# Kernel tuning notes

Hardware: AMD Instinct MI355X
Metric: run time of the kernel (lower is better)

## Reference

```python
import jax, jax.numpy as jnp
import numpy as np

N = 50000   # nodes
E = 800000  # edges (sparse adjacency nnz)
FI = 256    # input feature dim
FO = 64     # output feature dim per head
H = 8       # attention heads


def setup_inputs() -> dict:
    key = jax.random.key(0)
    ks = jax.random.split(key, 6)
    x = jax.random.normal(ks[0], (N, FI), dtype=jnp.float32)
    W = jax.random.normal(ks[1], (H, FI, FO), dtype=jnp.float32) * 0.05
    a = jax.random.normal(ks[2], (H, FO), dtype=jnp.float32) * 0.05
    b = jax.random.normal(ks[3], (H, FO), dtype=jnp.float32) * 0.05
    rows = jax.random.randint(ks[4], (E,), 0, N, dtype=jnp.int32)
    cols = jax.random.randint(ks[5], (E,), 0, N, dtype=jnp.int32)
    return {"x": x, "W": W, "a": a, "b": b, "rows": rows, "cols": cols}


def reference(x, W, a, b, rows, cols):
    # SparseGAT forward: per head linear -> edge scores -> sparse row softmax
    # -> sparse aggregation -> bias; heads averaged then ReLU.
    n = x.shape[0]
    h = W.shape[0]
    NEG_SLOPE = 0.2  # tf.nn.leaky_relu default alpha
    acc = None
    for i in range(h):  # small fixed loop over heads
        t = x @ W[i]                                   # [N, FO]
        aw = t @ a[i]                                  # [N]
        e = jax.nn.leaky_relu(aw[rows] + aw[cols], NEG_SLOPE)   # [E]
        # sparse softmax per row (segment softmax, numerically stable)
        m = jax.ops.segment_max(e, rows, num_segments=n)        # [N]
        ex = jnp.exp(e - m[rows])                                # [E]
        den = jax.ops.segment_sum(ex, rows, num_segments=n)      # [N]
        coef = ex / den[rows]                                    # [E]
        # sparse matmul: sum_j coef_ij * t_j
        agg = jax.ops.segment_sum(coef[:, None] * t[cols], rows, num_segments=n)
        agg = agg + b[i]
        acc = agg if acc is None else acc + agg
    return jax.nn.relu(acc / h)
```

## Files before the change

### kernel.cpp

```cpp
#include <hip/hip_runtime.h>
#include <hip/hip_bf16.h>


#define FI 256
#define FO 64
#define NH 8
#define FC (NH * FO)
#define TTP 528

typedef _Float16 f16x8 __attribute__((ext_vector_type(8)));
typedef float f32x16 __attribute__((ext_vector_type(16)));
typedef float f32x8 __attribute__((ext_vector_type(8)));

__global__ __launch_bounds__(256)
void p1_wconv(const float* __restrict__ W, _Float16* __restrict__ Wth) {
  int idx = blockIdx.x * 256 + threadIdx.x;
  if (idx >= NH * FO * FI) return;
  int k = idx & (FI - 1);
  int f = (idx >> 8) & (FO - 1);
  int h = idx >> 14;
  Wth[idx] = (_Float16)W[((size_t)h * FI + k) * FO + f];
}

__global__ __launch_bounds__(256)
void k1_fused(const float* __restrict__ x, const _Float16* __restrict__ Wth,
              const float* __restrict__ a, _Float16* __restrict__ Th2,
              float* __restrict__ aw, int N) {
  __shared__ _Float16 Xs[32][264];
  __shared__ _Float16 Tt[32][TTP];
  const int bm  = blockIdx.x * 32;
  const int t   = threadIdx.x;
  const int lane = t & 63;
  const int wid  = t >> 6;
  const int l31 = lane & 31;
  const int kh  = (lane >> 5) * 8;

  #pragma unroll
  for (int r = 0; r < 8; ++r) {
    int i = t + r * 256;
    int row = i >> 6;
    int q   = i & 63;
    int grow = bm + row;
    float4 v = make_float4(0.f, 0.f, 0.f, 0.f);
    if (grow < N)
      v = reinterpret_cast<const float4*>(&x[(size_t)grow * FI])[q];
    _Float16 o[4] = {(_Float16)v.x, (_Float16)v.y, (_Float16)v.z, (_Float16)v.w};
    *reinterpret_cast<uint2*>(&Xs[row][q * 4]) = *reinterpret_cast<uint2*>(o);
  }
  __syncthreads();

  #pragma unroll
  for (int hh = 0; hh < 2; ++hh) {
    const int h = wid * 2 + hh;
    #pragma unroll
    for (int wc = 0; wc < 2; ++wc) {
      const _Float16* Wcol = Wth + ((size_t)h * FO + wc * 32 + l31) * FI;
      f32x16 acc = (f32x16)0.0f;
      #pragma unroll
      for (int kk = 0; kk < 16; ++kk) {
        f16x8 af = *reinterpret_cast<const f16x8*>(&Xs[l31][kk * 16 + kh]);
        f16x8 bf = *reinterpret_cast<const f16x8*>(&Wcol[kk * 16 + kh]);
        acc = __builtin_amdgcn_mfma_f32_32x32x16_f16(af, bf, acc, 0, 0, 0);
      }
      const int f = wc * 32 + l31;
      #pragma unroll
      for (int reg = 0; reg < 16; ++reg) {
        int rr = (reg & 3) + 8 * (reg >> 2) + 4 * (lane >> 5);
        Tt[rr][f * NH + h] = (_Float16)acc[reg];
      }
    }
  }
  __syncthreads();

  float a_l[NH];
  #pragma unroll
  for (int h = 0; h < NH; ++h) a_l[h] = a[h * FO + lane];
  #pragma unroll
  for (int rr = 0; rr < 8; ++rr) {
    const int row = wid * 8 + rr;
    f16x8 v = *reinterpret_cast<const f16x8*>(&Tt[row][lane * NH]);
    float p[NH];
    #pragma unroll
    for (int h = 0; h < NH; ++h) p[h] = (float)v[h] * a_l[h];
    #pragma unroll
    for (int off = 1; off < 64; off <<= 1) {
      #pragma unroll
      for (int h = 0; h < NH; ++h) p[h] += __shfl_xor(p[h], off);
    }
    if (lane == 0 && bm + row < N) {
      f32x8 o;
      #pragma unroll
      for (int h = 0; h < NH; ++h) o[h] = p[h];
      *reinterpret_cast<f32x8*>(&aw[(size_t)(bm + row) * NH]) = o;
    }
  }

  #pragma unroll
  for (int r = 0; r < 8; ++r) {
    int i = t + r * 256;
    int row = i >> 6;
    int q   = i & 63;
    if (bm + row < N)
      reinterpret_cast<uint4*>(&Th2[(size_t)(bm + row) * FC])[q] =
          *reinterpret_cast<const uint4*>(&Tt[row][q * 8]);
  }
}

__global__ __launch_bounds__(256)
void b1_hist(const int* __restrict__ rows, int* __restrict__ deg, int E) {
  int e = blockIdx.x * 256 + threadIdx.x;
  if (e < E) atomicAdd(&deg[rows[e]], 1);
}

__global__ __launch_bounds__(256)
void b2a_blocksum(const int* __restrict__ deg, int* __restrict__ blocksums, int N) {
  __shared__ int red[256];
  const int t = threadIdx.x;
  const int base = blockIdx.x * 1024 + t * 4;
  int s = 0;
  #pragma unroll
  for (int j = 0; j < 4; ++j) { int i = base + j; if (i < N) s += deg[i]; }
  red[t] = s;
  __syncthreads();
  for (int off = 128; off; off >>= 1) {
    if (t < off) red[t] += red[t + off];
    __syncthreads();
  }
  if (t == 0) blocksums[blockIdx.x] = red[0];
}

__global__ __launch_bounds__(64)
void b2b_scanblocks(int* __restrict__ blocksums, int nb,
                    int* __restrict__ row_start, int N, int E) {
  const int lane = threadIdx.x;
  int carry = 0;
  for (int base = 0; base < nb; base += 64) {
    int i = base + lane;
    int v = (i < nb) ? blocksums[i] : 0;
    int inc = v;
    #pragma unroll
    for (int off = 1; off < 64; off <<= 1) {
      int t = __shfl_up(inc, off);
      if (lane >= off) inc += t;
    }
    if (i < nb) blocksums[i] = inc - v + carry;
    carry += __shfl(inc, 63);
  }
  if (lane == 0) row_start[N] = E;
}

__global__ __launch_bounds__(256)
void b2c_rescan(const int* __restrict__ deg, const int* __restrict__ blocksums,
                int* __restrict__ row_start, int* __restrict__ cursor, int N) {
  __shared__ int ts[256];
  const int t = threadIdx.x;
  const int base = blockIdx.x * 1024 + t * 4;
  int v[4]; int s = 0;
  #pragma unroll
  for (int j = 0; j < 4; ++j) { int i = base + j; v[j] = (i < N) ? deg[i] : 0; s += v[j]; }
  ts[t] = s;
  __syncthreads();
  for (int off = 1; off < 256; off <<= 1) {
    int add = (t >= off) ? ts[t - off] : 0;
    __syncthreads();
    ts[t] += add;
    __syncthreads();
  }
  int run = blocksums[blockIdx.x] + ts[t] - s;
  #pragma unroll
  for (int j = 0; j < 4; ++j) {
    int i = base + j;
    if (i < N) { row_start[i] = run; cursor[i] = run; run += v[j]; }
  }
}

__global__ __launch_bounds__(256)
void b3_scatter(const int* __restrict__ rows, const int* __restrict__ cols,
                int* __restrict__ cursor, int* __restrict__ colperm, int E) {
  int e = blockIdx.x * 256 + threadIdx.x;
  if (e >= E) return;
  int pos = atomicAdd(&cursor[rows[e]], 1);
  colperm[pos] = cols[e];
}

__global__ __launch_bounds__(256)
void k4_fused(const int* __restrict__ row_start, const int* __restrict__ colperm,
              const float* __restrict__ aw, const _Float16* __restrict__ Th2,
              const float* __restrict__ b, float* __restrict__ out, int N) {
  const int lane16 = threadIdx.x & 15;
  const int gbase  = threadIdx.x & 48;
  const int r = blockIdx.x * 16 + (threadIdx.x >> 4);
  if (r >= N) return;

  const int s0 = row_start[r], s1 = row_start[r + 1];

  f32x8 awr = *reinterpret_cast<const f32x8*>(&aw[(size_t)r * NH]);

  float facc[4][NH] = {};
  float dacc[NH] = {};

  for (int base = s0; base < s1; base += 16) {
    const int mm = min(16, s1 - base);
    const bool valid = lane16 < mm;
    int c_l = valid ? colperm[base + lane16] : 0;

    f32x8 awc = *reinterpret_cast<const f32x8*>(&aw[(size_t)c_l * NH]);
    float ex[NH];
    #pragma unroll
    for (int h = 0; h < NH; ++h) {
      float s = awr[h] + awc[h];
      float lr = s > 0.f ? s : 0.2f * s;
      ex[h] = valid ? __expf(lr) : 0.f;
      dacc[h] += ex[h];
    }

    for (int j = 0; j < mm; ++j) {
      int cj = __shfl(c_l, gbase + j);
      const _Float16* tp = Th2 + (size_t)cj * FC + lane16 * NH;
      f16x8 tv0 = *reinterpret_cast<const f16x8*>(tp);
      f16x8 tv1 = *reinterpret_cast<const f16x8*>(tp + 128);
      f16x8 tv2 = *reinterpret_cast<const f16x8*>(tp + 256);
      f16x8 tv3 = *reinterpret_cast<const f16x8*>(tp + 384);
      #pragma unroll
      for (int h = 0; h < NH; ++h) {
        float e = __shfl(ex[h], gbase + j);
        facc[0][h] = fmaf(e, (float)tv0[h], facc[0][h]);
        facc[1][h] = fmaf(e, (float)tv1[h], facc[1][h]);
        facc[2][h] = fmaf(e, (float)tv2[h], facc[2][h]);
        facc[3][h] = fmaf(e, (float)tv3[h], facc[3][h]);
      }
    }
  }

  #pragma unroll
  for (int h = 0; h < NH; ++h) {
    #pragma unroll
    for (int off = 1; off < 16; off <<= 1)
      dacc[h] += __shfl_xor(dacc[h], off);
  }

  float rden[NH];
  #pragma unroll
  for (int h = 0; h < NH; ++h) rden[h] = dacc[h] > 0.f ? 1.0f / dacc[h] : 0.f;

  #pragma unroll
  for (int q = 0; q < 4; ++q) {
    const int f = q * 16 + lane16;
    float sb = 0.f;
    #pragma unroll
    for (int h = 0; h < NH; ++h) sb += b[h * FO + f];
    float v = 0.f;
    #pragma unroll
    for (int h = 0; h < NH; ++h) v += facc[q][h] * rden[h];
    v = (v + sb) * 0.125f;
    out[(size_t)r * FO + f] = v > 0.f ? v : 0.f;
  }
}

extern "C" void kernel_launch(void* const* d_in, const int* in_sizes, int n_in,
                              void* d_out, int out_size, void* d_ws, size_t ws_size,
                              hipStream_t stream) {
  const float* x    = (const float*)d_in[0];
  const float* W    = (const float*)d_in[1];
  const float* a    = (const float*)d_in[2];
  const float* b    = (const float*)d_in[3];
  const int*   rows = (const int*)d_in[4];
  const int*   cols = (const int*)d_in[5];
  const int N = in_sizes[0] / FI;
  const int E = in_sizes[4];

  char* p = (char*)d_ws;
  _Float16* Th2      = (_Float16*)p;  p += (size_t)N * FC * sizeof(_Float16);
  _Float16* Wth      = (_Float16*)p;  p += (size_t)NH * FO * FI * sizeof(_Float16);
  float*    aw       = (float*)p;     p += (size_t)N * NH * sizeof(float);
  int*      deg      = (int*)p;       p += (size_t)N * sizeof(int);
  int*      row_start= (int*)p;       p += (size_t)(N + 4) * sizeof(int);
  int*      cursor   = (int*)p;       p += (size_t)N * sizeof(int);
  int*      colperm  = (int*)p;       p += (size_t)E * sizeof(int);
  int*      blocksums= (int*)p;       p += 64 * sizeof(int);
  float*    out = (float*)d_out;

  const int nb = (N + 1023) / 1024;

  hipMemsetAsync(deg, 0, (size_t)N * sizeof(int), stream);
  b1_hist<<<(E + 255) / 256, 256, 0, stream>>>(rows, deg, E);
  b2a_blocksum<<<nb, 256, 0, stream>>>(deg, blocksums, N);
  b2b_scanblocks<<<1, 64, 0, stream>>>(blocksums, nb, row_start, N, E);
  b2c_rescan<<<nb, 256, 0, stream>>>(deg, blocksums, row_start, cursor, N);
  b3_scatter<<<(E + 255) / 256, 256, 0, stream>>>(rows, cols, cursor, colperm, E);

  p1_wconv<<<(NH * FO * FI + 255) / 256, 256, 0, stream>>>(W, Wth);
  k1_fused<<<(N + 31) / 32, 256, 0, stream>>>(x, Wth, a, Th2, aw, N);

  k4_fused<<<(N + 15) / 16, 256, 0, stream>>>(row_start, colperm, aw, Th2, b, out, N);
}
```

Baseline: 314.6 us.

## Retile projection GEMM to 128-row blocks with per-head waves; prefetch gathers in aggregation

The projection kernel now handles 128 rows per block with 512 threads. Each wave owns one head and computes four 32-row MFMA tiles, so every W fragment load is reused across four row tiles, and K is staged in two halves to reduce shared memory. The attention logits come straight from the accumulators through lane shuffles rather than from an LDS re-read. The aggregation kernel stores edge exponentials in shared memory instead of shuffling them per head, and software-prefetches the next neighbour's feature row to hide gather latency, at the cost of more registers and extra LDS traffic.

New measurement: 292.6 us. 7.0% less time.

```diff
diff --git a/kernel.cpp b/kernel.cpp
--- a/kernel.cpp
+++ b/kernel.cpp
@@ -5,12 +5,13 @@
 #define FI 256
 #define FO 64
 #define NH 8
-#define FC (NH * FO)
-#define TTP 528
+#define FC 512
+#define BM 128
 
 typedef _Float16 f16x8 __attribute__((ext_vector_type(8)));
 typedef float f32x16 __attribute__((ext_vector_type(16)));
 typedef float f32x8 __attribute__((ext_vector_type(8)));
+typedef float f32x4 __attribute__((ext_vector_type(4)));
 
 __global__ __launch_bounds__(256)
 void p1_wconv(const float* __restrict__ W, _Float16* __restrict__ Wth) {
@@ -22,87 +23,97 @@
   Wth[idx] = (_Float16)W[((size_t)h * FI + k) * FO + f];
 }
 
-__global__ __launch_bounds__(256)
-void k1_fused(const float* __restrict__ x, const _Float16* __restrict__ Wth,
-              const float* __restrict__ a, _Float16* __restrict__ Th2,
-              float* __restrict__ aw, int N) {
-  __shared__ _Float16 Xs[32][264];
-  __shared__ _Float16 Tt[32][TTP];
-  const int bm  = blockIdx.x * 32;
-  const int t   = threadIdx.x;
+__global__ __launch_bounds__(512)
+void k1_v2(const float* __restrict__ x, const _Float16* __restrict__ Wth,
+           const float* __restrict__ a, _Float16* __restrict__ Th2,
+           float* __restrict__ aw, int N) {
+  __shared__ _Float16 smem[BM * 136];
+  auto Xs = reinterpret_cast<_Float16(*)[136]>(smem);
+  auto Tt = reinterpret_cast<_Float16(*)[512]>(smem);
+  const int bm = blockIdx.x * BM;
+  const int t = threadIdx.x;
+  const int w = t >> 6;
   const int lane = t & 63;
-  const int wid  = t >> 6;
   const int l31 = lane & 31;
-  const int kh  = (lane >> 5) * 8;
-
-  #pragma unroll
-  for (int r = 0; r < 8; ++r) {
-    int i = t + r * 256;
-    int row = i >> 6;
-    int q   = i & 63;
-    int grow = bm + row;
-    float4 v = make_float4(0.f, 0.f, 0.f, 0.f);
-    if (grow < N)
-      v = reinterpret_cast<const float4*>(&x[(size_t)grow * FI])[q];
-    _Float16 o[4] = {(_Float16)v.x, (_Float16)v.y, (_Float16)v.z, (_Float16)v.w};
-    *reinterpret_cast<uint2*>(&Xs[row][q * 4]) = *reinterpret_cast<uint2*>(o);
-  }
-  __syncthreads();
-
-  #pragma unroll
-  for (int hh = 0; hh < 2; ++hh) {
-    const int h = wid * 2 + hh;
+  const int kh = (lane >> 5) * 8;
+  const _Float16* Wh = Wth + (size_t)w * (FO * FI);
+
+  f32x16 acc[4][2];
+  #pragma unroll
+  for (int mr = 0; mr < 4; ++mr)
+    #pragma unroll
+    for (int wc = 0; wc < 2; ++wc) acc[mr][wc] = (f32x16)0.0f;
+
+  #pragma unroll
+  for (int k0 = 0; k0 < 2; ++k0) {
+    if (k0) __syncthreads();
+    #pragma unroll
+    for (int r = 0; r < 8; ++r) {
+      int i = t + r * 512;
+      int row = i >> 5;
+      int q = i & 31;
+      float4 v = make_float4(0.f, 0.f, 0.f, 0.f);
+      if (bm + row < N)
+        v = reinterpret_cast<const float4*>(&x[(size_t)(bm + row) * FI + k0 * 128])[q];
+      _Float16 o[4] = {(_Float16)v.x, (_Float16)v.y, (_Float16)v.z, (_Float16)v.w};
+      *reinterpret_cast<uint2*>(&Xs[row][q * 4]) = *reinterpret_cast<uint2*>(o);
+    }
+    __syncthreads();
+    #pragma unroll
+    for (int kk = 0; kk < 8; ++kk) {
+      f16x8 af[4], bf[2];
+      #pragma unroll
+      for (int mr = 0; mr < 4; ++mr)
+        af[mr] = *reinterpret_cast<const f16x8*>(&Xs[mr * 32 + l31][kk * 16 + kh]);
+      #pragma unroll
+      for (int wc = 0; wc < 2; ++wc)
+        bf[wc] = *reinterpret_cast<const f16x8*>(
+            &Wh[(size_t)(wc * 32 + l31) * FI + k0 * 128 + kk * 16 + kh]);
+      #pragma unroll
+      for (int mr = 0; mr < 4; ++mr)
+        #pragma unroll
+        for (int wc = 0; wc < 2; ++wc)
+          acc[mr][wc] =
+              __builtin_amdgcn_mfma_f32_32x32x16_f16(af[mr], bf[wc], acc[mr][wc], 0, 0, 0);
+    }
+  }
+
+  const float av0 = a[w * FO + l31], av1 = a[w * FO + 32 + l31];
+  #pragma unroll
+  for (int mr = 0; mr < 4; ++mr)
+    #pragma unroll
+    for (int reg = 0; reg < 16; ++reg) {
+      float s = acc[mr][0][reg] * av0 + acc[mr][1][reg] * av1;
+      #pragma unroll
+      for (int off = 1; off < 32; off <<= 1) s += __shfl_xor(s, off);
+      if (l31 == 0) {
+        int rl = mr * 32 + (reg & 3) + 8 * (reg >> 2) + 4 * (lane >> 5);
+        if (bm + rl < N) aw[(size_t)(bm + rl) * NH + w] = s;
+      }
+    }
+
+  #pragma unroll
+  for (int ch = 0; ch < 4; ++ch) {
+    __syncthreads();
     #pragma unroll
     for (int wc = 0; wc < 2; ++wc) {
-      const _Float16* Wcol = Wth + ((size_t)h * FO + wc * 32 + l31) * FI;
-      f32x16 acc = (f32x16)0.0f;
-      #pragma unroll
-      for (int kk = 0; kk < 16; ++kk) {
-        f16x8 af = *reinterpret_cast<const f16x8*>(&Xs[l31][kk * 16 + kh]);
-        f16x8 bf = *reinterpret_cast<const f16x8*>(&Wcol[kk * 16 + kh]);
-        acc = __builtin_amdgcn_mfma_f32_32x32x16_f16(af, bf, acc, 0, 0, 0);
+      const int f = wc * 32 + l31;
+      #pragma unroll
+      for (int reg = 0; reg < 16; ++reg) {
+        int rl = (reg & 3) + 8 * (reg >> 2) + 4 * (lane >> 5);
+        Tt[rl][f * NH + w] = (_Float16)acc[ch][wc][reg];
       }
-      const int f = wc * 32 + l31;
-      #pragma unroll
-      for (int reg = 0; reg < 16; ++reg) {
-        int rr = (reg & 3) + 8 * (reg >> 2) + 4 * (lane >> 5);
-        Tt[rr][f * NH + h] = (_Float16)acc[reg];
-      }
-    }
-  }
-  __syncthreads();
-
-  float a_l[NH];
-  #pragma unroll
-  for (int h = 0; h < NH; ++h) a_l[h] = a[h * FO + lane];
-  #pragma unroll
-  for (int rr = 0; rr < 8; ++rr) {
-    const int row = wid * 8 + rr;
-    f16x8 v = *reinterpret_cast<const f16x8*>(&Tt[row][lane * NH]);
-    float p[NH];
-    #pragma unroll
-    for (int h = 0; h < NH; ++h) p[h] = (float)v[h] * a_l[h];
-    #pragma unroll
-    for (int off = 1; off < 64; off <<= 1) {
-      #pragma unroll
-      for (int h = 0; h < NH; ++h) p[h] += __shfl_xor(p[h], off);
-    }
-    if (lane == 0 && bm + row < N) {
-      f32x8 o;
-      #pragma unroll
-      for (int h = 0; h < NH; ++h) o[h] = p[h];
-      *reinterpret_cast<f32x8*>(&aw[(size_t)(bm + row) * NH]) = o;
-    }
-  }
-
-  #pragma unroll
-  for (int r = 0; r < 8; ++r) {
-    int i = t + r * 256;
-    int row = i >> 6;
-    int q   = i & 63;
-    if (bm + row < N)
-      reinterpret_cast<uint4*>(&Th2[(size_t)(bm + row) * FC])[q] =
-          *reinterpret_cast<const uint4*>(&Tt[row][q * 8]);
+    }
+    __syncthreads();
+    #pragma unroll
+    for (int r = 0; r < 4; ++r) {
+      int i = t + r * 512;
+      int row = i >> 6, q = i & 63;
+      int grow = bm + ch * 32 + row;
+      if (grow < N)
+        *reinterpret_cast<uint4*>(&Th2[(size_t)grow * FC + q * 8]) =
+            *reinterpret_cast<const uint4*>(&Tt[row][q * 8]);
+    }
   }
 }
 
@@ -187,13 +198,15 @@
 void k4_fused(const int* __restrict__ row_start, const int* __restrict__ colperm,
               const float* __restrict__ aw, const _Float16* __restrict__ Th2,
               const float* __restrict__ b, float* __restrict__ out, int N) {
+  __shared__ float exs[16][132];
   const int lane16 = threadIdx.x & 15;
+  const int g      = threadIdx.x >> 4;
   const int gbase  = threadIdx.x & 48;
-  const int r = blockIdx.x * 16 + (threadIdx.x >> 4);
+  const int r = blockIdx.x * 16 + g;
   if (r >= N) return;
+  float* exg = &exs[g][0];
 
   const int s0 = row_start[r], s1 = row_start[r + 1];
-
   f32x8 awr = *reinterpret_cast<const f32x8*>(&aw[(size_t)r * NH]);
 
   float facc[4][NH] = {};
@@ -205,30 +218,45 @@
     int c_l = valid ? colperm[base + lane16] : 0;
 
     f32x8 awc = *reinterpret_cast<const f32x8*>(&aw[(size_t)c_l * NH]);
-    float ex[NH];
     #pragma unroll
     for (int h = 0; h < NH; ++h) {
       float s = awr[h] + awc[h];
       float lr = s > 0.f ? s : 0.2f * s;
-      ex[h] = valid ? __expf(lr) : 0.f;
-      dacc[h] += ex[h];
-    }
-
+      float e = valid ? __expf(lr) : 0.f;
+      dacc[h] += e;
+      exg[lane16 * NH + h] = e;
+    }
+
+    int cj = __shfl(c_l, gbase);
+    const _Float16* tp = Th2 + (size_t)cj * FC + lane16 * NH;
+    f16x8 A0 = *reinterpret_cast<const f16x8*>(tp);
+    f16x8 A1 = *reinterpret_cast<const f16x8*>(tp + 128);
+    f16x8 A2 = *reinterpret_cast<const f16x8*>(tp + 256);
+    f16x8 A3 = *reinterpret_cast<const f16x8*>(tp + 384);
     for (int j = 0; j < mm; ++j) {
-      int cj = __shfl(c_l, gbase + j);
-      const _Float16* tp = Th2 + (size_t)cj * FC + lane16 * NH;
-      f16x8 tv0 = *reinterpret_cast<const f16x8*>(tp);
-      f16x8 tv1 = *reinterpret_cast<const f16x8*>(tp + 128);
-      f16x8 tv2 = *reinterpret_cast<const f16x8*>(tp + 256);
-      f16x8 tv3 = *reinterpret_cast<const f16x8*>(tp + 384);
-      #pragma unroll
-      for (int h = 0; h < NH; ++h) {
-        float e = __shfl(ex[h], gbase + j);
-        facc[0][h] = fmaf(e, (float)tv0[h], facc[0][h]);
-        facc[1][h] = fmaf(e, (float)tv1[h], facc[1][h]);
-        facc[2][h] = fmaf(e, (float)tv2[h], facc[2][h]);
-        facc[3][h] = fmaf(e, (float)tv3[h], facc[3][h]);
+      f16x8 B0, B1, B2, B3;
+      if (j + 1 < mm) {
+        int cn = __shfl(c_l, gbase + j + 1);
+        const _Float16* tq = Th2 + (size_t)cn * FC + lane16 * NH;
+        B0 = *reinterpret_cast<const f16x8*>(tq);
+        B1 = *reinterpret_cast<const f16x8*>(tq + 128);
+        B2 = *reinterpret_cast<const f16x8*>(tq + 256);
+        B3 = *reinterpret_cast<const f16x8*>(tq + 384);
       }
+      f32x4 e0 = *reinterpret_cast<const f32x4*>(&exg[j * NH]);
+      f32x4 e1 = *reinterpret_cast<const f32x4*>(&exg[j * NH + 4]);
+      #pragma unroll
+      for (int h = 0; h < 4; ++h) {
+        facc[0][h]     = fmaf(e0[h], (float)A0[h],     facc[0][h]);
+        facc[1][h]     = fmaf(e0[h], (float)A1[h],     facc[1][h]);
+        facc[2][h]     = fmaf(e0[h], (float)A2[h],     facc[2][h]);
+        facc[3][h]     = fmaf(e0[h], (float)A3[h],     facc[3][h]);
+        facc[0][h + 4] = fmaf(e1[h], (float)A0[h + 4], facc[0][h + 4]);
+        facc[1][h + 4] = fmaf(e1[h], (float)A1[h + 4], facc[1][h + 4]);
+        facc[2][h + 4] = fmaf(e1[h], (float)A2[h + 4], facc[2][h + 4]);
+        facc[3][h + 4] = fmaf(e1[h], (float)A3[h + 4], facc[3][h + 4]);
+      }
+      A0 = B0; A1 = B1; A2 = B2; A3 = B3;
     }
   }
 
@@ -290,7 +318,7 @@
   b3_scatter<<<(E + 255) / 256, 256, 0, stream>>>(rows, cols, cursor, colperm, E);
 
   p1_wconv<<<(NH * FO * FI + 255) / 256, 256, 0, stream>>>(W, Wth);
-  k1_fused<<<(N + 31) / 32, 256, 0, stream>>>(x, Wth, a, Th2, aw, N);
+  k1_v2<<<(N + BM - 1) / BM, 512, 0, stream>>>(x, Wth, a, Th2, aw, N);
 
   k4_fused<<<(N + 15) / 16, 256, 0, stream>>>(row_start, colperm, aw, Th2, b, out, N);
 }
```
